# Kernel optimization log

Measured on AMD Instinct MI355X. Metric: run time of the kernel, lower is better.

Reference implementation:

```python
import jax, jax.numpy as jnp
import numpy as np

R = 5          # output_size of AdaptiveMaxPool1d (init default)
B = 2048       # batch
T = 8192       # padded max sequence length


def setup_inputs() -> dict:
    key = jax.random.key(0)
    k1, k2 = jax.random.split(key)
    inputs = jax.random.normal(k1, (B, T), dtype=jnp.float32)
    # lengths in [R, T] so each of the R adaptive windows is non-empty
    lengths = jax.random.randint(k2, (B,), R, T + 1)
    return {"inputs": inputs, "lengths": lengths}


def _minmax(inputs, lengths, r_out=R):
    """Vectorized ragged AdaptiveMaxPool1d(+min via -pool(-x)) then sort.

    PyTorch AdaptiveMaxPool1d window r over a length-L signal:
      start = floor(r*L/R), end = ceil((r+1)*L/R)
    """
    _, t_max = inputs.shape
    t = jnp.arange(t_max)              # [T]
    L = lengths[:, None]               # [B,1]
    pos_inf = jnp.asarray(jnp.inf, inputs.dtype)
    maxes, mins = [], []
    for r in range(r_out):             # fixed small loop over R windows
        start = (r * L) // r_out                       # [B,1]
        end = ((r + 1) * L + r_out - 1) // r_out       # [B,1], <= L
        mask = (t >= start) & (t < end)                # [B,T]
        maxes.append(jnp.max(jnp.where(mask, inputs, -pos_inf), axis=1))
        mins.append(jnp.min(jnp.where(mask, inputs, pos_inf), axis=1))
    out = jnp.stack(maxes + mins, axis=1)  # [B, 2R]: cat([top, neg]) per sample
    return jnp.sort(out, axis=1)           # ascending, like torch .sort()


def reference(inputs, lengths):
    return _minmax(inputs, lengths)
```

## Files before the change

kernel.cpp:

```cpp
#include <hip/hip_runtime.h>
#include <cfloat>

#define RWIN 5
#define TMAX 8192

__global__ __launch_bounds__(5 * 64) void minmax_sort_kernel(
    const float* __restrict__ in, const int* __restrict__ lengths,
    float* __restrict__ out)
{
    __shared__ float sm[2 * RWIN];

    const int b    = blockIdx.x;
    const int tid  = threadIdx.x;
    const int w    = tid >> 6;
    const int lane = tid & 63;

    const int L = lengths[b];
    const float* rowp = in + (size_t)b * TMAX;

    const int s = (w * L) / RWIN;
    const int e = ((w + 1) * L + (RWIN - 1)) / RWIN;

    float mx = -__builtin_inff();
    float mn =  __builtin_inff();

    int s4 = (s + 3) & ~3; if (s4 > e)  s4 = e;
    int e4 = e & ~3;       if (e4 < s4) e4 = s4;

    for (int t = s + lane; t < s4; t += 64) {
        const float x = rowp[t];
        mx = fmaxf(mx, x); mn = fminf(mn, x);
    }
    for (int t = s4 + lane * 4; t < e4; t += 64 * 4) {
        const float4 v = *reinterpret_cast<const float4*>(rowp + t);
        mx = fmaxf(mx, fmaxf(fmaxf(v.x, v.y), fmaxf(v.z, v.w)));
        mn = fminf(mn, fminf(fminf(v.x, v.y), fminf(v.z, v.w)));
    }
    for (int t = e4 + lane; t < e; t += 64) {
        const float x = rowp[t];
        mx = fmaxf(mx, x); mn = fminf(mn, x);
    }

    #pragma unroll
    for (int off = 1; off < 64; off <<= 1) {
        mx = fmaxf(mx, __shfl_xor(mx, off));
        mn = fminf(mn, __shfl_xor(mn, off));
    }
    if (lane == 0) { sm[w] = mx; sm[RWIN + w] = mn; }
    __syncthreads();

    if (tid < 2 * RWIN) {
        const float v = sm[tid];
        int pos = 0;
        #pragma unroll
        for (int j = 0; j < 2 * RWIN; ++j) {
            const float vj = sm[j];
            pos += (int)((vj < v) | ((vj == v) & (j < tid)));
        }
        out[b * (2 * RWIN) + pos] = v;
    }
}

extern "C" void kernel_launch(void* const* d_in, const int* in_sizes, int n_in,
                              void* d_out, int out_size, void* d_ws, size_t ws_size,
                              hipStream_t stream) {
    const float* in      = (const float*)d_in[0];
    const int*   lengths = (const int*)d_in[1];
    float*       out     = (float*)d_out;
    const int B = in_sizes[1];
    minmax_sort_kernel<<<B, 5 * 64, 0, stream>>>(in, lengths, out);
}
```

Measured before the change: 12.77 us.

## Split work into per-window reduction blocks plus separate rank-sort kernel

Launches one 128-thread block per (row, window) pair instead of one 320-thread block per row. Partial max/min go to a workspace buffer, and a second kernel does the rank sort per row. The goal is better load balance and more parallelism over the memory-bound reduction. The cost is an extra kernel launch and a round trip through global memory for the workspace.

```diff
diff --git a/kernel.cpp b/kernel.cpp
--- a/kernel.cpp
+++ b/kernel.cpp
@@ -1,25 +1,26 @@
 #include <hip/hip_runtime.h>
-#include <cfloat>
 
 #define RWIN 5
 #define TMAX 8192
 
-__global__ __launch_bounds__(5 * 64) void minmax_sort_kernel(
+__global__ __launch_bounds__(128) void window_minmax_kernel(
     const float* __restrict__ in, const int* __restrict__ lengths,
-    float* __restrict__ out)
+    float* __restrict__ ws)
 {
-    __shared__ float sm[2 * RWIN];
+    __shared__ float sm[4];
 
-    const int b    = blockIdx.x;
+    const int task = blockIdx.x;
+    const int row  = task / RWIN;
+    const int win  = task % RWIN;
     const int tid  = threadIdx.x;
     const int w    = tid >> 6;
     const int lane = tid & 63;
 
-    const int L = lengths[b];
-    const float* rowp = in + (size_t)b * TMAX;
+    const int L = lengths[row];
+    const float* rowp = in + (size_t)row * TMAX;
 
-    const int s = (w * L) / RWIN;
-    const int e = ((w + 1) * L + (RWIN - 1)) / RWIN;
+    const int s = (win * L) / RWIN;
+    const int e = ((win + 1) * L + (RWIN - 1)) / RWIN;
 
     float mx = -__builtin_inff();
     float mn =  __builtin_inff();
@@ -27,16 +28,16 @@
     int s4 = (s + 3) & ~3; if (s4 > e)  s4 = e;
     int e4 = e & ~3;       if (e4 < s4) e4 = s4;
 
-    for (int t = s + lane; t < s4; t += 64) {
+    for (int t = s + tid; t < s4; t += 128) {
         const float x = rowp[t];
         mx = fmaxf(mx, x); mn = fminf(mn, x);
     }
-    for (int t = s4 + lane * 4; t < e4; t += 64 * 4) {
+    for (int t = s4 + tid * 4; t < e4; t += 128 * 4) {
         const float4 v = *reinterpret_cast<const float4*>(rowp + t);
         mx = fmaxf(mx, fmaxf(fmaxf(v.x, v.y), fmaxf(v.z, v.w)));
         mn = fminf(mn, fminf(fminf(v.x, v.y), fminf(v.z, v.w)));
     }
-    for (int t = e4 + lane; t < e; t += 64) {
+    for (int t = e4 + tid; t < e; t += 128) {
         const float x = rowp[t];
         mx = fmaxf(mx, x); mn = fminf(mn, x);
     }
@@ -46,19 +47,30 @@
         mx = fmaxf(mx, __shfl_xor(mx, off));
         mn = fminf(mn, __shfl_xor(mn, off));
     }
-    if (lane == 0) { sm[w] = mx; sm[RWIN + w] = mn; }
+    if (lane == 0) { sm[w] = mx; sm[2 + w] = mn; }
     __syncthreads();
+    if (tid == 0) {
+        ws[row * (2 * RWIN) + win]        = fmaxf(sm[0], sm[1]);
+        ws[row * (2 * RWIN) + RWIN + win] = fminf(sm[2], sm[3]);
+    }
+}
 
-    if (tid < 2 * RWIN) {
-        const float v = sm[tid];
-        int pos = 0;
-        #pragma unroll
-        for (int j = 0; j < 2 * RWIN; ++j) {
-            const float vj = sm[j];
-            pos += (int)((vj < v) | ((vj == v) & (j < tid)));
-        }
-        out[b * (2 * RWIN) + pos] = v;
+__global__ __launch_bounds__(256) void rank_sort_kernel(
+    const float* __restrict__ ws, float* __restrict__ out, int n)
+{
+    const int g = blockIdx.x * 256 + threadIdx.x;
+    if (g >= n) return;
+    const int row = g / (2 * RWIN);
+    const int j   = g % (2 * RWIN);
+    const float* base = ws + row * (2 * RWIN);
+    const float v = base[j];
+    int pos = 0;
+    #pragma unroll
+    for (int k = 0; k < 2 * RWIN; ++k) {
+        const float vk = base[k];
+        pos += (int)((vk < v) | ((vk == v) & (k < j)));
     }
+    out[row * (2 * RWIN) + pos] = v;
 }
 
 extern "C" void kernel_launch(void* const* d_in, const int* in_sizes, int n_in,
@@ -67,6 +79,11 @@
     const float* in      = (const float*)d_in[0];
     const int*   lengths = (const int*)d_in[1];
     float*       out     = (float*)d_out;
+    float*       ws      = (float*)d_ws;
     const int B = in_sizes[1];
-    minmax_sort_kernel<<<B, 5 * 64, 0, stream>>>(in, lengths, out);
+
+    window_minmax_kernel<<<B * RWIN, 128, 0, stream>>>(in, lengths, ws);
+
+    const int n = B * 2 * RWIN;
+    rank_sort_kernel<<<(n + 255) / 256, 256, 0, stream>>>(ws, out, n);
 }
```

Result: slower. 15.10 us (+18.2%).

## Use two waves per window with masked aligned float4 loads

Applied to the files above, without the earlier changes.

Doubles the block to 640 threads so each adaptive window is reduced by two wavefronts instead of one. The scalar head and tail loops are replaced by a single aligned float4 loop that masks out-of-window elements, and the loop is unrolled by 4. The per-wave partials are combined through an extra shared-memory stage and barrier, and the length is made wave-uniform with readfirstlane. The aim is more memory parallelism per row and less divergent scalar edge work, at the cost of an extra sync and per-element compare/select work.

```diff
diff --git a/kernel.cpp b/kernel.cpp
--- a/kernel.cpp
+++ b/kernel.cpp
@@ -1,44 +1,46 @@
 #include <hip/hip_runtime.h>
-#include <cfloat>
 
 #define RWIN 5
 #define TMAX 8192
 
-__global__ __launch_bounds__(5 * 64) void minmax_sort_kernel(
+__global__ __launch_bounds__(640) void minmax_sort_kernel(
     const float* __restrict__ in, const int* __restrict__ lengths,
     float* __restrict__ out)
 {
-    __shared__ float sm[2 * RWIN];
+    __shared__ float smx[2 * RWIN];
+    __shared__ float smn[2 * RWIN];
+    __shared__ float vals[2 * RWIN];
 
     const int b    = blockIdx.x;
     const int tid  = threadIdx.x;
-    const int w    = tid >> 6;
+    const int win  = tid >> 7;
+    const int t2   = tid & 127;
+    const int wid  = tid >> 6;
     const int lane = tid & 63;
 
-    const int L = lengths[b];
+    const int L = __builtin_amdgcn_readfirstlane(lengths[b]);
     const float* rowp = in + (size_t)b * TMAX;
 
-    const int s = (w * L) / RWIN;
-    const int e = ((w + 1) * L + (RWIN - 1)) / RWIN;
+    const int s  = (win * L) / RWIN;
+    const int e  = ((win + 1) * L + (RWIN - 1)) / RWIN;
+    const int sa = s & ~3;
 
-    float mx = -__builtin_inff();
-    float mn =  __builtin_inff();
+    const float NINF = -__builtin_inff();
+    const float PINF =  __builtin_inff();
+    float mx = NINF;
+    float mn = PINF;
 
-    int s4 = (s + 3) & ~3; if (s4 > e)  s4 = e;
-    int e4 = e & ~3;       if (e4 < s4) e4 = s4;
-
-    for (int t = s + lane; t < s4; t += 64) {
-        const float x = rowp[t];
-        mx = fmaxf(mx, x); mn = fminf(mn, x);
-    }
-    for (int t = s4 + lane * 4; t < e4; t += 64 * 4) {
+    #pragma unroll 4
+    for (int t = sa + t2 * 4; t < e; t += 128 * 4) {
         const float4 v = *reinterpret_cast<const float4*>(rowp + t);
-        mx = fmaxf(mx, fmaxf(fmaxf(v.x, v.y), fmaxf(v.z, v.w)));
-        mn = fminf(mn, fminf(fminf(v.x, v.y), fminf(v.z, v.w)));
-    }
-    for (int t = e4 + lane; t < e; t += 64) {
-        const float x = rowp[t];
-        mx = fmaxf(mx, x); mn = fminf(mn, x);
+        const float xs[4] = {v.x, v.y, v.z, v.w};
+        #pragma unroll
+        for (int j = 0; j < 4; ++j) {
+            const int  idx = t + j;
+            const bool ok  = (idx >= s) & (idx < e);
+            mx = fmaxf(mx, ok ? xs[j] : NINF);
+            mn = fminf(mn, ok ? xs[j] : PINF);
+        }
     }
 
     #pragma unroll
@@ -46,15 +48,23 @@
         mx = fmaxf(mx, __shfl_xor(mx, off));
         mn = fminf(mn, __shfl_xor(mn, off));
     }
-    if (lane == 0) { sm[w] = mx; sm[RWIN + w] = mn; }
+    if (lane == 0) { smx[wid] = mx; smn[wid] = mn; }
+    __syncthreads();
+
+    if (tid < RWIN) {
+        vals[tid] = fmaxf(smx[2 * tid], smx[2 * tid + 1]);
+    } else if (tid < 2 * RWIN) {
+        const int k = tid - RWIN;
+        vals[tid] = fminf(smn[2 * k], smn[2 * k + 1]);
+    }
     __syncthreads();
 
     if (tid < 2 * RWIN) {
-        const float v = sm[tid];
+        const float v = vals[tid];
         int pos = 0;
         #pragma unroll
         for (int j = 0; j < 2 * RWIN; ++j) {
-            const float vj = sm[j];
+            const float vj = vals[j];
             pos += (int)((vj < v) | ((vj == v) & (j < tid)));
         }
         out[b * (2 * RWIN) + pos] = v;
@@ -68,5 +78,5 @@
     const int*   lengths = (const int*)d_in[1];
     float*       out     = (float*)d_out;
     const int B = in_sizes[1];
-    minmax_sort_kernel<<<B, 5 * 64, 0, stream>>>(in, lengths, out);
+    minmax_sort_kernel<<<B, 640, 0, stream>>>(in, lengths, out);
 }
```

After: 15.63 us. 1.22x slower.
